# Performance work log

Hardware: AMD Instinct MI355X
Metric: run time of the kernel (lower is better)

Reference implementation:

```python
import jax, jax.numpy as jnp
import numpy as np

H = 16  # num_attention_heads
LN_EPS = 1e-12


def setup_inputs() -> dict:
    key = jax.random.key(0)
    ks = jax.random.split(key, 13)
    S, B, D = 2048, 2, 1024
    std = 0.02
    return {
        "query_tensor": jax.random.normal(ks[0], (S, B, D), jnp.float32),
        "key_tensor": jax.random.normal(ks[1], (S, B, D), jnp.float32),
        "value_tensor": jax.random.normal(ks[2], (S, B, D), jnp.float32),
        "Wq": jax.random.normal(ks[3], (D, D), jnp.float32) * std,
        "bq": jnp.zeros((D,), jnp.float32),
        "Wk": jax.random.normal(ks[4], (D, D), jnp.float32) * std,
        "bk": jnp.zeros((D,), jnp.float32),
        "Wv": jax.random.normal(ks[5], (D, D), jnp.float32) * std,
        "bv": jnp.zeros((D,), jnp.float32),
        "Wo": jax.random.normal(ks[6], (D, D), jnp.float32) * std,
        "bo": jnp.zeros((D,), jnp.float32),
        "ln_w": jnp.ones((D,), jnp.float32),
        "ln_b": jnp.zeros((D,), jnp.float32),
    }


def _layernorm(x, w, b):
    u = jnp.mean(x, axis=-1, keepdims=True)
    s = jnp.mean(jnp.square(x - u), axis=-1, keepdims=True)
    return w * ((x - u) / jnp.sqrt(s + LN_EPS)) + b


def reference(query_tensor, key_tensor, value_tensor, Wq, bq, Wk, bk, Wv, bv, Wo, bo, ln_w, ln_b):
    S, B, D = query_tensor.shape
    dh = D // H
    # QKV projections (nn.Linear: x @ W.T + b)
    q = query_tensor @ Wq.T + bq          # (S, B, D)
    k = key_tensor @ Wk.T + bk            # (Sk, B, D)
    v = value_tensor @ Wv.T + bv          # (Sk, B, D)
    # (S, B, D) -> (B*H, S, dh)
    q = q.reshape(S, B * H, dh).transpose(1, 0, 2)
    k = k.reshape(-1, B * H, dh).transpose(1, 0, 2)
    v = v.reshape(-1, B * H, dh).transpose(1, 0, 2)
    # NOTE: original code has NO 1/sqrt(dh) scaling
    scores = jnp.einsum('nqd,nkd->nqk', q, k)            # (B*H, S, Sk)
    probs = jax.nn.softmax(scores, axis=-1)
    # dropout is identity in eval mode
    ctx = jnp.einsum('nqk,nkd->nqd', probs, v)           # (B*H, S, dh)
    ctx = ctx.transpose(1, 0, 2).reshape(S, B, D)
    # BertSelfOutput: dense + residual + LayerNorm (dropout identity)
    out = ctx @ Wo.T + bo
    return _layernorm(out + query_tensor, ln_w, ln_b)
```

## Files before the change

### kernel.cpp

```cpp
#include <hip/hip_runtime.h>

#define SEQ    2048
#define BATCH  2
#define DMODEL 1024
#define NHEAD  16
#define DH     64
#define MROWS  (SEQ*BATCH)
#define RS     (BATCH*DMODEL)
#define LN_EPS 1e-12f

typedef __attribute__((ext_vector_type(8))) short short8;
typedef __attribute__((ext_vector_type(4))) float floatx4;

#define AS_GLOBAL __attribute__((address_space(1)))
#define AS_LDS    __attribute__((address_space(3)))

__device__ __forceinline__ float bf2f(unsigned short s) {
    union { unsigned u; float f; } a; a.u = ((unsigned)s) << 16; return a.f;
}
__device__ __forceinline__ unsigned short f2bf(float x) {
    union { float f; unsigned u; } a; a.f = x;
    unsigned r = a.u + 0x7fffu + ((a.u >> 16) & 1u);
    return (unsigned short)(r >> 16);
}
__device__ __forceinline__ uint4 cvt8(const float* __restrict__ p) {
    float4 x0 = *(const float4*)(p);
    float4 x1 = *(const float4*)(p + 4);
    union { uint4 u; unsigned short s[8]; } r;
    r.s[0] = f2bf(x0.x); r.s[1] = f2bf(x0.y);
    r.s[2] = f2bf(x0.z); r.s[3] = f2bf(x0.w);
    r.s[4] = f2bf(x1.x); r.s[5] = f2bf(x1.y);
    r.s[6] = f2bf(x1.z); r.s[7] = f2bf(x1.w);
    return r.u;
}

__global__ void beacon_kernel(float* out, float val) {
    if (threadIdx.x == 0) out[0] = val;
}

__global__ __launch_bounds__(256)
void cvt_kernel(const float* __restrict__ s0, const float* __restrict__ s1,
                const float* __restrict__ s2, const float* __restrict__ s3,
                const float* __restrict__ s4, const float* __restrict__ s5,
                const float* __restrict__ s6,
                unsigned short* __restrict__ d0, unsigned short* __restrict__ d1,
                unsigned short* __restrict__ d2, unsigned short* __restrict__ d3,
                unsigned short* __restrict__ d4, unsigned short* __restrict__ d5,
                unsigned short* __restrict__ d6)
{
    const float* srcs[7] = {s0, s1, s2, s3, s4, s5, s6};
    unsigned short* dsts[7] = {d0, d1, d2, d3, d4, d5, d6};
    const int cnts[7] = {4194304, 4194304, 4194304, 1048576, 1048576, 1048576, 1048576};
    const int z = blockIdx.z;
    const float* src = srcs[z];
    unsigned short* dst = dsts[z];
    const int count = cnts[z];
    const int stride = gridDim.x * 256 * 8;
    for (int i = (blockIdx.x * 256 + threadIdx.x) * 8; i < count; i += stride)
        *(uint4*)&dst[i] = cvt8(&src[i]);
}

__global__ __launch_bounds__(256)
void vt_kernel(const unsigned short* __restrict__ Vb,
               unsigned short* __restrict__ VT)
{
    __shared__ __align__(16) short T[64*72];
    const int tid = threadIdx.x;
    const int s0 = blockIdx.x * 64;
    const int bh = blockIdx.y;
    const int b = bh >> 4, h = bh & 15;

    #pragma unroll
    for (int rep = 0; rep < 2; ++rep) {
        int c = tid + rep * 256;
        int s = c >> 3, cc = c & 7;
        *(uint4*)&T[s*72 + cc*8] =
            *(const uint4*)&Vb[((s0 + s) * BATCH + b) * DMODEL + h*64 + cc*8];
    }
    __syncthreads();
    #pragma unroll
    for (int rep = 0; rep < 2; ++rep) {
        int o = tid + rep * 256;
        int d = o >> 3, sc = o & 7;
        union { uint4 u; unsigned short e[8]; } pk;
        #pragma unroll
        for (int j = 0; j < 8; ++j)
            pk.e[j] = (unsigned short)T[(sc*8 + j)*72 + d];
        *(uint4*)&VT[bh*(DH*SEQ) + d*SEQ + s0 + sc*8] = pk.u;
    }
}

template<int OUTF32>
__device__ __forceinline__ void gemm_bf16_body(
    const unsigned short* __restrict__ A,
    const unsigned short* __restrict__ W,
    const float* __restrict__ bias,
    void* __restrict__ Cout)
{
    __shared__ __align__(16) short Alds[128*32];
    __shared__ __align__(16) short Blds[128*32];

    const int tid  = threadIdx.x;
    const int lane = tid & 63;
    const int wave = tid >> 6;
    const int lrow = lane & 15;
    const int lq   = lane >> 4;
    const int m0 = blockIdx.x * 128;
    const int n0 = blockIdx.y * 128;
    const int mw = (wave >> 1) * 64;
    const int nw = (wave & 1) * 64;
    const int K  = DMODEL;

    const int chunk0 = tid;
    const int chunk1 = tid + 256;
    const int row0 = chunk0 >> 2, col0 = (chunk0 & 3) << 3;
    const int row1 = chunk1 >> 2, col1 = (chunk1 & 3) << 3;
    const unsigned short* gA0 = &A[(m0 + row0) * K + col0];
    const unsigned short* gA1 = &A[(m0 + row1) * K + col1];
    const unsigned short* gB0 = &W[(n0 + row0) * K + col0];
    const unsigned short* gB1 = &W[(n0 + row1) * K + col1];
    AS_LDS unsigned int* lA0 = (AS_LDS unsigned int*)&Alds[(wave*64)*8];
    AS_LDS unsigned int* lA1 = (AS_LDS unsigned int*)&Alds[(256 + wave*64)*8];
    AS_LDS unsigned int* lB0 = (AS_LDS unsigned int*)&Blds[(wave*64)*8];
    AS_LDS unsigned int* lB1 = (AS_LDS unsigned int*)&Blds[(256 + wave*64)*8];

    floatx4 zero = {0.f, 0.f, 0.f, 0.f};
    floatx4 acc[4][4];
    #pragma unroll
    for (int i = 0; i < 4; ++i)
        #pragma unroll
        for (int j = 0; j < 4; ++j) acc[i][j] = zero;

    for (int k0 = 0; k0 < K; k0 += 32) {
        __builtin_amdgcn_global_load_lds((const AS_GLOBAL unsigned int*)(gA0 + k0), lA0, 16, 0, 0);
        __builtin_amdgcn_global_load_lds((const AS_GLOBAL unsigned int*)(gA1 + k0), lA1, 16, 0, 0);
        __builtin_amdgcn_global_load_lds((const AS_GLOBAL unsigned int*)(gB0 + k0), lB0, 16, 0, 0);
        __builtin_amdgcn_global_load_lds((const AS_GLOBAL unsigned int*)(gB1 + k0), lB1, 16, 0, 0);
        __syncthreads();
        short8 af[4], bfg[4];
        #pragma unroll
        for (int mi = 0; mi < 4; ++mi)
            af[mi] = *(const short8*)&Alds[(mw + mi*16 + lrow)*32 + lq*8];
        #pragma unroll
        for (int ni = 0; ni < 4; ++ni)
            bfg[ni] = *(const short8*)&Blds[(nw + ni*16 + lrow)*32 + lq*8];
        #pragma unroll
        for (int mi = 0; mi < 4; ++mi)
            #pragma unroll
            for (int ni = 0; ni < 4; ++ni)
                acc[mi][ni] = __builtin_amdgcn_mfma_f32_16x16x32_bf16(af[mi], bfg[ni], acc[mi][ni], 0, 0, 0);
        __syncthreads();
    }

    #pragma unroll
    for (int mi = 0; mi < 4; ++mi) {
        #pragma unroll
        for (int ni = 0; ni < 4; ++ni) {
            int n = n0 + nw + ni*16 + lrow;
            float bv_ = bias[n];
            #pragma unroll
            for (int r = 0; r < 4; ++r) {
                int m = m0 + mw + mi*16 + lq*4 + r;
                float v = acc[mi][ni][r] + bv_;
                if (OUTF32) ((float*)Cout)[m * DMODEL + n] = v;
                else ((unsigned short*)Cout)[m * DMODEL + n] = f2bf(v);
            }
        }
    }
}

__global__ __launch_bounds__(256)
void qkv_bf16(const unsigned short* __restrict__ qb, const unsigned short* __restrict__ kb,
              const unsigned short* __restrict__ vb,
              const unsigned short* __restrict__ Wqb, const float* __restrict__ bq,
              const unsigned short* __restrict__ Wkb, const float* __restrict__ bk,
              const unsigned short* __restrict__ Wvb, const float* __restrict__ bv,
              unsigned short* __restrict__ Qo, unsigned short* __restrict__ Ko,
              unsigned short* __restrict__ Vo)
{
    const unsigned short *A, *W; const float* B; unsigned short* C;
    if (blockIdx.z == 0)      { A = qb; W = Wqb; B = bq; C = Qo; }
    else if (blockIdx.z == 1) { A = kb; W = Wkb; B = bk; C = Ko; }
    else                      { A = vb; W = Wvb; B = bv; C = Vo; }
    gemm_bf16_body<0>(A, W, B, C);
}

__global__ __launch_bounds__(256)
void oproj_bf16(const unsigned short* __restrict__ Cx,
                const unsigned short* __restrict__ Wob, const float* __restrict__ bo,
                float* __restrict__ O32)
{
    gemm_bf16_body<1>(Cx, Wob, bo, O32);
}

__global__ __launch_bounds__(256)
void qkv_mfma(const float* __restrict__ q_in, const float* __restrict__ k_in,
              const float* __restrict__ v_in,
              const float* __restrict__ Wq, const float* __restrict__ bq,
              const float* __restrict__ Wk, const float* __restrict__ bk,
              const float* __restrict__ Wv, const float* __restrict__ bv,
              unsigned short* __restrict__ Qo, unsigned short* __restrict__ Ko,
              unsigned short* __restrict__ Vo)
{
    const float *A, *W, *B; unsigned short* C;
    if (blockIdx.z == 0)      { A = q_in; W = Wq; B = bq; C = Qo; }
    else if (blockIdx.z == 1) { A = k_in; W = Wk; B = bk; C = Ko; }
    else                      { A = v_in; W = Wv; B = bv; C = Vo; }

    __shared__ __align__(16) short Alds[128*32];
    __shared__ __align__(16) short Blds[128*32];
    const int tid  = threadIdx.x;
    const int lane = tid & 63;
    const int wave = tid >> 6;
    const int lrow = lane & 15;
    const int lq   = lane >> 4;
    const int m0 = blockIdx.x * 128;
    const int n0 = blockIdx.y * 128;
    const int mw = (wave >> 1) * 64;
    const int nw = (wave & 1) * 64;
    const int K  = DMODEL;

    floatx4 zero = {0.f, 0.f, 0.f, 0.f};
    floatx4 acc[4][4];
    #pragma unroll
    for (int i = 0; i < 4; ++i)
        #pragma unroll
        for (int j = 0; j < 4; ++j) acc[i][j] = zero;

    for (int k0 = 0; k0 < K; k0 += 32) {
        #pragma unroll
        for (int rep = 0; rep < 2; ++rep) {
            int chunk = tid + rep * 256;
            int row = chunk >> 2;
            int col = (chunk & 3) << 3;
            *(uint4*)&Alds[row*32 + col] = cvt8(&A[(m0 + row) * K + k0 + col]);
            *(uint4*)&Blds[row*32 + col] = cvt8(&W[(n0 + row) * K + k0 + col]);
        }
        __syncthreads();
        short8 af[4], bfg[4];
        #pragma unroll
        for (int mi = 0; mi < 4; ++mi)
            af[mi] = *(const short8*)&Alds[(mw + mi*16 + lrow)*32 + lq*8];
        #pragma unroll
        for (int ni = 0; ni < 4; ++ni)
            bfg[ni] = *(const short8*)&Blds[(nw + ni*16 + lrow)*32 + lq*8];
        #pragma unroll
        for (int mi = 0; mi < 4; ++mi)
            #pragma unroll
            for (int ni = 0; ni < 4; ++ni)
                acc[mi][ni] = __builtin_amdgcn_mfma_f32_16x16x32_bf16(af[mi], bfg[ni], acc[mi][ni], 0, 0, 0);
        __syncthreads();
    }

    #pragma unroll
    for (int mi = 0; mi < 4; ++mi) {
        #pragma unroll
        for (int ni = 0; ni < 4; ++ni) {
            int n = n0 + nw + ni*16 + lrow;
            float bv_ = B[n];
            #pragma unroll
            for (int r = 0; r < 4; ++r) {
                int m = m0 + mw + mi*16 + lq*4 + r;
                C[m * DMODEL + n] = f2bf(acc[mi][ni][r] + bv_);
            }
        }
    }
}

__global__ __launch_bounds__(256)
void oproj_mfma(const unsigned short* __restrict__ Cx,
                const float* __restrict__ Wo, const float* __restrict__ bo,
                float* __restrict__ O32)
{
    __shared__ __align__(16) short Alds[128*32];
    __shared__ __align__(16) short Blds[128*32];
    const int tid  = threadIdx.x;
    const int lane = tid & 63;
    const int wave = tid >> 6;
    const int lrow = lane & 15;
    const int lq   = lane >> 4;
    const int m0 = blockIdx.x * 128;
    const int n0 = blockIdx.y * 128;
    const int mw = (wave >> 1) * 64;
    const int nw = (wave & 1) * 64;
    const int K  = DMODEL;

    floatx4 zero = {0.f, 0.f, 0.f, 0.f};
    floatx4 acc[4][4];
    #pragma unroll
    for (int i = 0; i < 4; ++i)
        #pragma unroll
        for (int j = 0; j < 4; ++j) acc[i][j] = zero;

    for (int k0 = 0; k0 < K; k0 += 32) {
        #pragma unroll
        for (int rep = 0; rep < 2; ++rep) {
            int chunk = tid + rep * 256;
            int row = chunk >> 2;
            int col = (chunk & 3) << 3;
            *(uint4*)&Alds[row*32 + col] = *(const uint4*)&Cx[(m0 + row) * K + k0 + col];
            *(uint4*)&Blds[row*32 + col] = cvt8(&Wo[(n0 + row) * K + k0 + col]);
        }
        __syncthreads();
        short8 af[4], bfg[4];
        #pragma unroll
        for (int mi = 0; mi < 4; ++mi)
            af[mi] = *(const short8*)&Alds[(mw + mi*16 + lrow)*32 + lq*8];
        #pragma unroll
        for (int ni = 0; ni < 4; ++ni)
            bfg[ni] = *(const short8*)&Blds[(nw + ni*16 + lrow)*32 + lq*8];
        #pragma unroll
        for (int mi = 0; mi < 4; ++mi)
            #pragma unroll
            for (int ni = 0; ni < 4; ++ni)
                acc[mi][ni] = __builtin_amdgcn_mfma_f32_16x16x32_bf16(af[mi], bfg[ni], acc[mi][ni], 0, 0, 0);
        __syncthreads();
    }

    #pragma unroll
    for (int mi = 0; mi < 4; ++mi) {
        #pragma unroll
        for (int ni = 0; ni < 4; ++ni) {
            int n = n0 + nw + ni*16 + lrow;
            float bv_ = bo[n];
            #pragma unroll
            for (int r = 0; r < 4; ++r) {
                int m = m0 + mw + mi*16 + lq*4 + r;
                O32[m * DMODEL + n] = acc[mi][ni][r] + bv_;
            }
        }
    }
}

__global__ __launch_bounds__(256)
void attn_mfma3(const unsigned short* __restrict__ Q,
                const unsigned short* __restrict__ Kg,
                const unsigned short* __restrict__ VT,
                unsigned short* __restrict__ Ctx)
{
    __shared__ __align__(16) short Qs[64*64];
    __shared__ __align__(16) short Ks[64*64];
    __shared__ __align__(16) short Vt[64*64];
    __shared__ __align__(16) short Ps[4][16*72];

    const int tid  = threadIdx.x;
    const int lane = tid & 63;
    const int wave = tid >> 6;
    const int lrow = lane & 15;
    const int lq   = lane >> 4;

    const int q0 = blockIdx.x * 64;
    const int bh = blockIdx.y;
    const int off = (bh >> 4) * DMODEL + (bh & 15) * DH;
    const unsigned short* VTb = VT + bh * (DH * SEQ);

    #pragma unroll
    for (int rep = 0; rep < 2; ++rep) {
        int c = rep*256 + wave*64 + lane;
        int r = c >> 3, cc = c & 7;
        const unsigned short* g = &Q[(q0 + r) * RS + off + ((cc ^ (r & 7)) << 3)];
        AS_LDS unsigned int* l = (AS_LDS unsigned int*)&Qs[(rep*256 + wave*64) * 8];
        __builtin_amdgcn_global_load_lds((const AS_GLOBAL unsigned int*)g, l, 16, 0, 0);
    }
    __syncthreads();

    short8 qf[2];
    #pragma unroll
    for (int ks = 0; ks < 2; ++ks) {
        int r = wave*16 + lrow;
        int cc = ks*4 + lq;
        qf[ks] = *(const short8*)&Qs[r*64 + ((cc ^ (r & 7)) << 3)];
    }

    floatx4 zero = {0.f, 0.f, 0.f, 0.f};
    float m_i = -1e30f, l_i = 0.f;
    floatx4 oacc[4];
    #pragma unroll
    for (int ni = 0; ni < 4; ++ni) oacc[ni] = zero;

    for (int kt = 0; kt < SEQ/64; ++kt) {
        __syncthreads();
        const int kbase = kt * 64;
        #pragma unroll
        for (int rep = 0; rep < 2; ++rep) {
            int c = rep*256 + wave*64 + lane;
            int r = c >> 3, cc = c & 7;
            int sw = ((cc ^ (r & 7)) << 3);
            const unsigned short* gk = &Kg[(kbase + r) * RS + off + sw];
            const unsigned short* gv = &VTb[r * SEQ + kbase + sw];
            AS_LDS unsigned int* lk = (AS_LDS unsigned int*)&Ks[(rep*256 + wave*64) * 8];
            AS_LDS unsigned int* lv = (AS_LDS unsigned int*)&Vt[(rep*256 + wave*64) * 8];
            __builtin_amdgcn_global_load_lds((const AS_GLOBAL unsigned int*)gk, lk, 16, 0, 0);
            __builtin_amdgcn_global_load_lds((const AS_GLOBAL unsigned int*)gv, lv, 16, 0, 0);
        }
        __syncthreads();

        floatx4 sacc[4];
        #pragma unroll
        for (int ni = 0; ni < 4; ++ni) sacc[ni] = zero;
        #pragma unroll
        for (int ni = 0; ni < 4; ++ni) {
            #pragma unroll
            for (int ks = 0; ks < 2; ++ks) {
                int key = ni*16 + lrow;
                int cc  = ks*4 + lq;
                short8 kf = *(const short8*)&Ks[key*64 + ((cc ^ (key & 7)) << 3)];
                sacc[ni] = __builtin_amdgcn_mfma_f32_16x16x32_bf16(kf, qf[ks], sacc[ni], 0, 0, 0);
            }
        }

        float mx = sacc[0][0];
        #pragma unroll
        for (int ni = 0; ni < 4; ++ni)
            #pragma unroll
            for (int r = 0; r < 4; ++r) mx = fmaxf(mx, sacc[ni][r]);
        mx = fmaxf(mx, __shfl_xor(mx, 16));
        mx = fmaxf(mx, __shfl_xor(mx, 32));
        float mnew = fmaxf(m_i, mx);
        float alpha = __expf(m_i - mnew);
        float p[4][4];
        float psum = 0.f;
        #pragma unroll
        for (int ni = 0; ni < 4; ++ni)
            #pragma unroll
            for (int r = 0; r < 4; ++r) {
                p[ni][r] = __expf(sacc[ni][r] - mnew);
                psum += p[ni][r];
            }
        psum += __shfl_xor(psum, 16);
        psum += __shfl_xor(psum, 32);
        l_i = l_i * alpha + psum;
        m_i = mnew;
        #pragma unroll
        for (int ni = 0; ni < 4; ++ni)
            #pragma unroll
            for (int r = 0; r < 4; ++r) oacc[ni][r] *= alpha;

        #pragma unroll
        for (int ni = 0; ni < 4; ++ni) {
            uint2 pk;
            pk.x = (unsigned)f2bf(p[ni][0]) | ((unsigned)f2bf(p[ni][1]) << 16);
            pk.y = (unsigned)f2bf(p[ni][2]) | ((unsigned)f2bf(p[ni][3]) << 16);
            *(uint2*)&Ps[wave][lrow*72 + ni*16 + lq*4] = pk;
        }
        __builtin_amdgcn_wave_barrier();

        short8 pf[2];
        #pragma unroll
        for (int ks = 0; ks < 2; ++ks)
            pf[ks] = *(const short8*)&Ps[wave][lrow*72 + ks*32 + lq*8];
        #pragma unroll
        for (int ni = 0; ni < 4; ++ni) {
            #pragma unroll
            for (int ks = 0; ks < 2; ++ks) {
                int d  = ni*16 + lrow;
                int cc = ks*4 + lq;
                short8 vf = *(const short8*)&Vt[d*64 + ((cc ^ (d & 7)) << 3)];
                oacc[ni] = __builtin_amdgcn_mfma_f32_16x16x32_bf16(vf, pf[ks], oacc[ni], 0, 0, 0);
            }
        }
    }

    const float inv = 1.f / l_i;
    const int q = q0 + wave*16 + lrow;
    #pragma unroll
    for (int ni = 0; ni < 4; ++ni) {
        uint2 ok;
        ok.x = (unsigned)f2bf(oacc[ni][0] * inv) | ((unsigned)f2bf(oacc[ni][1] * inv) << 16);
        ok.y = (unsigned)f2bf(oacc[ni][2] * inv) | ((unsigned)f2bf(oacc[ni][3] * inv) << 16);
        *(uint2*)&Ctx[q * RS + off + ni*16 + lq*4] = ok;
    }
}

__global__ __launch_bounds__(256)
void attn_mfma2(const unsigned short* __restrict__ Q,
                const unsigned short* __restrict__ Kg,
                const unsigned short* __restrict__ V,
                unsigned short* __restrict__ Ctx)
{
    __shared__ __align__(16) short Qs[64*72];
    __shared__ __align__(16) short Ks[64*72];
    __shared__ __align__(16) short Vt[64*72];
    __shared__ __align__(16) short Ps[4][16*72];

    const int tid  = threadIdx.x;
    const int lane = tid & 63;
    const int wave = tid >> 6;
    const int lrow = lane & 15;
    const int lq   = lane >> 4;

    const int q0 = blockIdx.x * 64;
    const int bh = blockIdx.y;
    const int off = (bh >> 4) * DMODEL + (bh & 15) * DH;

    #pragma unroll
    for (int rep = 0; rep < 2; ++rep) {
        int chunk = tid + rep * 256;
        int r = chunk >> 3;
        int c = (chunk & 7) << 3;
        *(uint4*)&Qs[r*72 + c] = *(const uint4*)&Q[(q0 + r) * RS + off + c];
    }
    __syncthreads();

    short8 qf[2];
    #pragma unroll
    for (int ks = 0; ks < 2; ++ks)
        qf[ks] = *(const short8*)&Qs[(wave*16 + lrow)*72 + ks*32 + lq*8];

    floatx4 zero = {0.f, 0.f, 0.f, 0.f};
    float m_i = -1e30f, l_i = 0.f;
    floatx4 oacc[4];
    #pragma unroll
    for (int ni = 0; ni < 4; ++ni) oacc[ni] = zero;

    for (int kt = 0; kt < SEQ/64; ++kt) {
        __syncthreads();
        const int kbase = kt * 64;
        #pragma unroll
        for (int rep = 0; rep < 2; ++rep) {
            int chunk = tid + rep * 256;
            int r = chunk >> 3;
            int c = (chunk & 7) << 3;
            *(uint4*)&Ks[r*72 + c] = *(const uint4*)&Kg[(kbase + r) * RS + off + c];
            uint4 vv = *(const uint4*)&V[(kbase + r) * RS + off + c];
            union { uint4 u; short s[8]; } uv; uv.u = vv;
            int swz = (chunk & 7) << 3;
            #pragma unroll
            for (int j = 0; j < 8; ++j)
                Vt[(c + j)*72 + (r ^ swz)] = uv.s[j];
        }
        __syncthreads();

        floatx4 sacc[4];
        #pragma unroll
        for (int ni = 0; ni < 4; ++ni) sacc[ni] = zero;
        #pragma unroll
        for (int ni = 0; ni < 4; ++ni) {
            #pragma unroll
            for (int ks = 0; ks < 2; ++ks) {
                short8 kf = *(const short8*)&Ks[(ni*16 + lrow)*72 + ks*32 + lq*8];
                sacc[ni] = __builtin_amdgcn_mfma_f32_16x16x32_bf16(kf, qf[ks], sacc[ni], 0, 0, 0);
            }
        }

        float mx = sacc[0][0];
        #pragma unroll
        for (int ni = 0; ni < 4; ++ni)
            #pragma unroll
            for (int r = 0; r < 4; ++r) mx = fmaxf(mx, sacc[ni][r]);
        mx = fmaxf(mx, __shfl_xor(mx, 16));
        mx = fmaxf(mx, __shfl_xor(mx, 32));
        float mnew = fmaxf(m_i, mx);
        float alpha = __expf(m_i - mnew);
        float p[4][4];
        float psum = 0.f;
        #pragma unroll
        for (int ni = 0; ni < 4; ++ni)
            #pragma unroll
            for (int r = 0; r < 4; ++r) {
                p[ni][r] = __expf(sacc[ni][r] - mnew);
                psum += p[ni][r];
            }
        psum += __shfl_xor(psum, 16);
        psum += __shfl_xor(psum, 32);
        l_i = l_i * alpha + psum;
        m_i = mnew;
        #pragma unroll
        for (int ni = 0; ni < 4; ++ni)
            #pragma unroll
            for (int r = 0; r < 4; ++r) oacc[ni][r] *= alpha;

        #pragma unroll
        for (int ni = 0; ni < 4; ++ni) {
            uint2 pk;
            pk.x = (unsigned)f2bf(p[ni][0]) | ((unsigned)f2bf(p[ni][1]) << 16);
            pk.y = (unsigned)f2bf(p[ni][2]) | ((unsigned)f2bf(p[ni][3]) << 16);
            *(uint2*)&Ps[wave][lrow*72 + ni*16 + lq*4] = pk;
        }
        __builtin_amdgcn_wave_barrier();

        short8 pf[2];
        #pragma unroll
        for (int ks = 0; ks < 2; ++ks)
            pf[ks] = *(const short8*)&Ps[wave][lrow*72 + ks*32 + lq*8];
        #pragma unroll
        for (int ni = 0; ni < 4; ++ni) {
            #pragma unroll
            for (int ks = 0; ks < 2; ++ks) {
                int d  = ni*16 + lrow;
                int kk = ks*32 + lq*8;
                int swz = ((d >> 3) & 7) << 3;
                short8 vf = *(const short8*)&Vt[d*72 + (kk ^ swz)];
                oacc[ni] = __builtin_amdgcn_mfma_f32_16x16x32_bf16(vf, pf[ks], oacc[ni], 0, 0, 0);
            }
        }
    }

    const float inv = 1.f / l_i;
    const int q = q0 + wave*16 + lrow;
    #pragma unroll
    for (int ni = 0; ni < 4; ++ni) {
        uint2 ok;
        ok.x = (unsigned)f2bf(oacc[ni][0] * inv) | ((unsigned)f2bf(oacc[ni][1] * inv) << 16);
        ok.y = (unsigned)f2bf(oacc[ni][2] * inv) | ((unsigned)f2bf(oacc[ni][3] * inv) << 16);
        *(uint2*)&Ctx[q * RS + off + ni*16 + lq*4] = ok;
    }
}

__global__ __launch_bounds__(256)
void ln2_kernel(const float* __restrict__ O,
                const float* __restrict__ resid,
                const float* __restrict__ w,
                const float* __restrict__ bb,
                float* __restrict__ out)
{
    __shared__ float r1[256];
    __shared__ float r2[256];
    const int row = blockIdx.x;
    const int tid = threadIdx.x;
    const int c4 = tid * 4;

    float4 o4 = *(const float4*)&O[row * DMODEL + c4];
    float4 q4 = *(const float4*)&resid[row * DMODEL + c4];
    float x0 = o4.x + q4.x;
    float x1 = o4.y + q4.y;
    float x2 = o4.z + q4.z;
    float x3 = o4.w + q4.w;

    r1[tid] = x0 + x1 + x2 + x3;
    r2[tid] = x0*x0 + x1*x1 + x2*x2 + x3*x3;
    __syncthreads();
    for (int st = 128; st > 0; st >>= 1) {
        if (tid < st) { r1[tid] += r1[tid + st]; r2[tid] += r2[tid + st]; }
        __syncthreads();
    }
    const float mean = r1[0] * (1.f / DMODEL);
    float var = r2[0] * (1.f / DMODEL) - mean * mean;
    var = fmaxf(var, 0.f);
    const float rstd = rsqrtf(var + LN_EPS);

    float4 w4 = *(const float4*)&w[c4];
    float4 b4 = *(const float4*)&bb[c4];
    float4 y;
    y.x = w4.x * ((x0 - mean) * rstd) + b4.x;
    y.y = w4.y * ((x1 - mean) * rstd) + b4.y;
    y.z = w4.z * ((x2 - mean) * rstd) + b4.z;
    y.w = w4.w * ((x3 - mean) * rstd) + b4.w;
    *(float4*)&out[row * DMODEL + c4] = y;
}

extern "C" void kernel_launch(void* const* d_in, const int* in_sizes, int n_in,
                              void* d_out, int out_size, void* d_ws, size_t ws_size,
                              hipStream_t stream) {
    const float* q_in = (const float*)d_in[0];
    const float* k_in = (const float*)d_in[1];
    const float* v_in = (const float*)d_in[2];
    const float* Wq = (const float*)d_in[3];  const float* bq = (const float*)d_in[4];
    const float* Wk = (const float*)d_in[5];  const float* bk = (const float*)d_in[6];
    const float* Wv = (const float*)d_in[7];  const float* bv = (const float*)d_in[8];
    const float* Wo = (const float*)d_in[9];  const float* bo = (const float*)d_in[10];
    const float* lnw = (const float*)d_in[11]; const float* lnb = (const float*)d_in[12];

    char* wsb = (char*)d_ws;
    unsigned short* QCtx = (unsigned short*)d_out;
    float*          outF = (float*)d_out;
    dim3 blk(256);

    if (ws_size >= (48u << 20)) {
        unsigned short* qb  = (unsigned short*)(wsb);
        unsigned short* kb  = (unsigned short*)(wsb + (8u  << 20));
        unsigned short* vb  = (unsigned short*)(wsb + (16u << 20));
        unsigned short* Wqb = (unsigned short*)(wsb + (24u << 20));
        unsigned short* Wkb = (unsigned short*)(wsb + (26u << 20));
        unsigned short* Wvb = (unsigned short*)(wsb + (28u << 20));
        unsigned short* Wob = (unsigned short*)(wsb + (30u << 20));
        unsigned short* Kb  = (unsigned short*)(wsb + (32u << 20));
        unsigned short* Vb  = (unsigned short*)(wsb + (40u << 20));
        unsigned short* VT  = (unsigned short*)(wsb);
        float*          O32 = (float*)(wsb);

        cvt_kernel<<<dim3(512, 1, 7), blk, 0, stream>>>(
            q_in, k_in, v_in, Wq, Wk, Wv, Wo,
            qb, kb, vb, Wqb, Wkb, Wvb, Wob);
        qkv_bf16<<<dim3(MROWS/128, DMODEL/128, 3), blk, 0, stream>>>(
            qb, kb, vb, Wqb, bq, Wkb, bk, Wvb, bv, QCtx, Kb, Vb);
        vt_kernel<<<dim3(SEQ/64, BATCH*NHEAD), blk, 0, stream>>>(Vb, VT);
        attn_mfma3<<<dim3(SEQ/64, BATCH*NHEAD), blk, 0, stream>>>(QCtx, Kb, VT, QCtx);
        oproj_bf16<<<dim3(MROWS/128, DMODEL/128), blk, 0, stream>>>(QCtx, Wob, bo, O32);
        ln2_kernel<<<dim3(MROWS), blk, 0, stream>>>(O32, q_in, lnw, lnb, outF);
    } else if (ws_size >= (16u << 20)) {
        unsigned short* Kb  = (unsigned short*)(wsb);
        unsigned short* Vb  = (unsigned short*)(wsb + (8u << 20));
        float*          O32 = (float*)(wsb);
        qkv_mfma<<<dim3(MROWS/128, DMODEL/128, 3), blk, 0, stream>>>(
            q_in, k_in, v_in, Wq, bq, Wk, bk, Wv, bv, QCtx, Kb, Vb);
        attn_mfma2<<<dim3(SEQ/64, BATCH*NHEAD), blk, 0, stream>>>(QCtx, Kb, Vb, QCtx);
        oproj_mfma<<<dim3(MROWS/128, DMODEL/128), blk, 0, stream>>>(QCtx, Wo, bo, O32);
        ln2_kernel<<<dim3(MROWS), blk, 0, stream>>>(O32, q_in, lnw, lnb, outF);
    } else {
        beacon_kernel<<<1, 64, 0, stream>>>((float*)d_out, 300.0f);
    }
}
```

Before: 271.1 us.

## Double-buffer K/V tiles in attention with lazy softmax rescale and shuffle LayerNorm

The attention kernel now double-buffers K and V^T tiles in LDS and prefetches the next tile before computing on the current one, leaving one barrier per iteration. This is meant to hide global-load latency behind the MFMA work. It also loads Q fragments straight from global memory and skips the online-softmax rescale unless the running max grows by more than 8. It further uses the hardware packed bf16 convert, swizzles the P scratch buffer, and raises wave priority around the MFMA blocks. LayerNorm replaces its LDS tree reduction with wave shuffles; the trade-offs are more LDS per block (about 40KB) and exp values up to e^8 before normalisation.

```diff
diff --git a/kernel.cpp b/kernel.cpp
--- a/kernel.cpp
+++ b/kernel.cpp
@@ -22,6 +22,11 @@
     union { float f; unsigned u; } a; a.f = x;
     unsigned r = a.u + 0x7fffu + ((a.u >> 16) & 1u);
     return (unsigned short)(r >> 16);
+}
+__device__ __forceinline__ unsigned cvt_pk_bf16(float a, float b) {
+    unsigned r;
+    asm("v_cvt_pk_bf16_f32 %0, %1, %2" : "=v"(r) : "v"(a), "v"(b));
+    return r;
 }
 __device__ __forceinline__ uint4 cvt8(const float* __restrict__ p) {
     float4 x0 = *(const float4*)(p);
@@ -333,15 +338,12 @@
 }
 
 __global__ __launch_bounds__(256)
-void attn_mfma3(const unsigned short* __restrict__ Q,
+void attn_mfma4(const unsigned short* __restrict__ Q,
                 const unsigned short* __restrict__ Kg,
                 const unsigned short* __restrict__ VT,
                 unsigned short* __restrict__ Ctx)
 {
-    __shared__ __align__(16) short Qs[64*64];
-    __shared__ __align__(16) short Ks[64*64];
-    __shared__ __align__(16) short Vt[64*64];
-    __shared__ __align__(16) short Ps[4][16*72];
+    __shared__ __align__(16) short SMEM[20480];
 
     const int tid  = threadIdx.x;
     const int lane = tid & 63;
@@ -353,24 +355,32 @@
     const int bh = blockIdx.y;
     const int off = (bh >> 4) * DMODEL + (bh & 15) * DH;
     const unsigned short* VTb = VT + bh * (DH * SEQ);
-
-    #pragma unroll
-    for (int rep = 0; rep < 2; ++rep) {
-        int c = rep*256 + wave*64 + lane;
-        int r = c >> 3, cc = c & 7;
-        const unsigned short* g = &Q[(q0 + r) * RS + off + ((cc ^ (r & 7)) << 3)];
-        AS_LDS unsigned int* l = (AS_LDS unsigned int*)&Qs[(rep*256 + wave*64) * 8];
-        __builtin_amdgcn_global_load_lds((const AS_GLOBAL unsigned int*)g, l, 16, 0, 0);
-    }
-    __syncthreads();
-
+    short* const psw = &SMEM[16384 + wave * 1024];
+
+    auto stageKV = [&](int kt, int b) {
+        const int kbase = kt * 64;
+        short* ksb = &SMEM[b * 8192];
+        short* vtb = &SMEM[b * 8192 + 4096];
+        #pragma unroll
+        for (int rep = 0; rep < 2; ++rep) {
+            int c = rep*256 + tid;
+            int r = c >> 3, cc = c & 7;
+            int sw = ((cc ^ (r & 7)) << 3);
+            __builtin_amdgcn_global_load_lds(
+                (const AS_GLOBAL unsigned int*)&Kg[(kbase + r) * RS + off + sw],
+                (AS_LDS unsigned int*)&ksb[(rep*256 + wave*64) * 8], 16, 0, 0);
+            __builtin_amdgcn_global_load_lds(
+                (const AS_GLOBAL unsigned int*)&VTb[r * SEQ + kbase + sw],
+                (AS_LDS unsigned int*)&vtb[(rep*256 + wave*64) * 8], 16, 0, 0);
+        }
+    };
+
+    stageKV(0, 0);
+
+    const int qrow = q0 + wave*16 + lrow;
     short8 qf[2];
-    #pragma unroll
-    for (int ks = 0; ks < 2; ++ks) {
-        int r = wave*16 + lrow;
-        int cc = ks*4 + lq;
-        qf[ks] = *(const short8*)&Qs[r*64 + ((cc ^ (r & 7)) << 3)];
-    }
+    qf[0] = *(const short8*)&Q[qrow * RS + off + lq*8];
+    qf[1] = *(const short8*)&Q[qrow * RS + off + 32 + lq*8];
 
     floatx4 zero = {0.f, 0.f, 0.f, 0.f};
     float m_i = -1e30f, l_i = 0.f;
@@ -378,36 +388,29 @@
     #pragma unroll
     for (int ni = 0; ni < 4; ++ni) oacc[ni] = zero;
 
+    __syncthreads();
+
     for (int kt = 0; kt < SEQ/64; ++kt) {
-        __syncthreads();
-        const int kbase = kt * 64;
-        #pragma unroll
-        for (int rep = 0; rep < 2; ++rep) {
-            int c = rep*256 + wave*64 + lane;
-            int r = c >> 3, cc = c & 7;
-            int sw = ((cc ^ (r & 7)) << 3);
-            const unsigned short* gk = &Kg[(kbase + r) * RS + off + sw];
-            const unsigned short* gv = &VTb[r * SEQ + kbase + sw];
-            AS_LDS unsigned int* lk = (AS_LDS unsigned int*)&Ks[(rep*256 + wave*64) * 8];
-            AS_LDS unsigned int* lv = (AS_LDS unsigned int*)&Vt[(rep*256 + wave*64) * 8];
-            __builtin_amdgcn_global_load_lds((const AS_GLOBAL unsigned int*)gk, lk, 16, 0, 0);
-            __builtin_amdgcn_global_load_lds((const AS_GLOBAL unsigned int*)gv, lv, 16, 0, 0);
-        }
-        __syncthreads();
+        const int cur = kt & 1;
+        if (kt + 1 < SEQ/64) stageKV(kt + 1, cur ^ 1);
+        const short* ksb = &SMEM[cur * 8192];
+        const short* vtb = &SMEM[cur * 8192 + 4096];
 
         floatx4 sacc[4];
         #pragma unroll
         for (int ni = 0; ni < 4; ++ni) sacc[ni] = zero;
-        #pragma unroll
-        for (int ni = 0; ni < 4; ++ni) {
-            #pragma unroll
-            for (int ks = 0; ks < 2; ++ks) {
+        __builtin_amdgcn_s_setprio(1);
+        #pragma unroll
+        for (int ni = 0; ni < 4; ++ni) {
+            #pragma unroll
+            for (int kk = 0; kk < 2; ++kk) {
                 int key = ni*16 + lrow;
-                int cc  = ks*4 + lq;
-                short8 kf = *(const short8*)&Ks[key*64 + ((cc ^ (key & 7)) << 3)];
-                sacc[ni] = __builtin_amdgcn_mfma_f32_16x16x32_bf16(kf, qf[ks], sacc[ni], 0, 0, 0);
-            }
-        }
+                int cc  = kk*4 + lq;
+                short8 kf = *(const short8*)&ksb[key*64 + ((cc ^ (key & 7)) << 3)];
+                sacc[ni] = __builtin_amdgcn_mfma_f32_16x16x32_bf16(kf, qf[kk], sacc[ni], 0, 0, 0);
+            }
+        }
+        __builtin_amdgcn_s_setprio(0);
 
         float mx = sacc[0][0];
         #pragma unroll
@@ -416,59 +419,71 @@
             for (int r = 0; r < 4; ++r) mx = fmaxf(mx, sacc[ni][r]);
         mx = fmaxf(mx, __shfl_xor(mx, 16));
         mx = fmaxf(mx, __shfl_xor(mx, 32));
-        float mnew = fmaxf(m_i, mx);
-        float alpha = __expf(m_i - mnew);
+        if (!__all(mx <= m_i + 8.f)) {
+            float mnew = fmaxf(m_i, mx);
+            float alpha = __expf(m_i - mnew);
+            l_i *= alpha;
+            #pragma unroll
+            for (int ni = 0; ni < 4; ++ni)
+                #pragma unroll
+                for (int r = 0; r < 4; ++r) oacc[ni][r] *= alpha;
+            m_i = mnew;
+        }
         float p[4][4];
         float psum = 0.f;
         #pragma unroll
         for (int ni = 0; ni < 4; ++ni)
             #pragma unroll
             for (int r = 0; r < 4; ++r) {
-                p[ni][r] = __expf(sacc[ni][r] - mnew);
+                p[ni][r] = __expf(sacc[ni][r] - m_i);
                 psum += p[ni][r];
             }
         psum += __shfl_xor(psum, 16);
         psum += __shfl_xor(psum, 32);
-        l_i = l_i * alpha + psum;
-        m_i = mnew;
-        #pragma unroll
-        for (int ni = 0; ni < 4; ++ni)
-            #pragma unroll
-            for (int r = 0; r < 4; ++r) oacc[ni][r] *= alpha;
+        l_i += psum;
 
         #pragma unroll
         for (int ni = 0; ni < 4; ++ni) {
             uint2 pk;
-            pk.x = (unsigned)f2bf(p[ni][0]) | ((unsigned)f2bf(p[ni][1]) << 16);
-            pk.y = (unsigned)f2bf(p[ni][2]) | ((unsigned)f2bf(p[ni][3]) << 16);
-            *(uint2*)&Ps[wave][lrow*72 + ni*16 + lq*4] = pk;
+            pk.x = cvt_pk_bf16(p[ni][0], p[ni][1]);
+            pk.y = cvt_pk_bf16(p[ni][2], p[ni][3]);
+            int t  = ni*2 + (lq >> 1);
+            int tp = t ^ (lrow & 7);
+            *(uint2*)&psw[lrow*64 + tp*8 + (lq & 1)*4] = pk;
         }
         __builtin_amdgcn_wave_barrier();
 
         short8 pf[2];
         #pragma unroll
-        for (int ks = 0; ks < 2; ++ks)
-            pf[ks] = *(const short8*)&Ps[wave][lrow*72 + ks*32 + lq*8];
-        #pragma unroll
-        for (int ni = 0; ni < 4; ++ni) {
-            #pragma unroll
-            for (int ks = 0; ks < 2; ++ks) {
+        for (int kk = 0; kk < 2; ++kk) {
+            int t  = kk*4 + lq;
+            int tp = t ^ (lrow & 7);
+            pf[kk] = *(const short8*)&psw[lrow*64 + tp*8];
+        }
+
+        __builtin_amdgcn_s_setprio(1);
+        #pragma unroll
+        for (int ni = 0; ni < 4; ++ni) {
+            #pragma unroll
+            for (int kk = 0; kk < 2; ++kk) {
                 int d  = ni*16 + lrow;
-                int cc = ks*4 + lq;
-                short8 vf = *(const short8*)&Vt[d*64 + ((cc ^ (d & 7)) << 3)];
-                oacc[ni] = __builtin_amdgcn_mfma_f32_16x16x32_bf16(vf, pf[ks], oacc[ni], 0, 0, 0);
-            }
-        }
+                int cc = kk*4 + lq;
+                short8 vf = *(const short8*)&vtb[d*64 + ((cc ^ (d & 7)) << 3)];
+                oacc[ni] = __builtin_amdgcn_mfma_f32_16x16x32_bf16(vf, pf[kk], oacc[ni], 0, 0, 0);
+            }
+        }
+        __builtin_amdgcn_s_setprio(0);
+
+        __syncthreads();
     }
 
     const float inv = 1.f / l_i;
-    const int q = q0 + wave*16 + lrow;
     #pragma unroll
     for (int ni = 0; ni < 4; ++ni) {
         uint2 ok;
-        ok.x = (unsigned)f2bf(oacc[ni][0] * inv) | ((unsigned)f2bf(oacc[ni][1] * inv) << 16);
-        ok.y = (unsigned)f2bf(oacc[ni][2] * inv) | ((unsigned)f2bf(oacc[ni][3] * inv) << 16);
-        *(uint2*)&Ctx[q * RS + off + ni*16 + lq*4] = ok;
+        ok.x = cvt_pk_bf16(oacc[ni][0] * inv, oacc[ni][1] * inv);
+        ok.y = cvt_pk_bf16(oacc[ni][2] * inv, oacc[ni][3] * inv);
+        *(uint2*)&Ctx[qrow * RS + off + ni*16 + lq*4] = ok;
     }
 }
 
@@ -614,8 +629,8 @@
                 const float* __restrict__ bb,
                 float* __restrict__ out)
 {
-    __shared__ float r1[256];
-    __shared__ float r2[256];
+    __shared__ float r1s[4];
+    __shared__ float r2s[4];
     const int row = blockIdx.x;
     const int tid = threadIdx.x;
     const int c4 = tid * 4;
@@ -627,15 +642,20 @@
     float x2 = o4.z + q4.z;
     float x3 = o4.w + q4.w;
 
-    r1[tid] = x0 + x1 + x2 + x3;
-    r2[tid] = x0*x0 + x1*x1 + x2*x2 + x3*x3;
+    float s1 = x0 + x1 + x2 + x3;
+    float s2 = x0*x0 + x1*x1 + x2*x2 + x3*x3;
+    #pragma unroll
+    for (int o = 32; o > 0; o >>= 1) {
+        s1 += __shfl_xor(s1, o);
+        s2 += __shfl_xor(s2, o);
+    }
+    if ((tid & 63) == 0) { r1s[tid >> 6] = s1; r2s[tid >> 6] = s2; }
     __syncthreads();
-    for (int st = 128; st > 0; st >>= 1) {
-        if (tid < st) { r1[tid] += r1[tid + st]; r2[tid] += r2[tid + st]; }
-        __syncthreads();
-    }
-    const float mean = r1[0] * (1.f / DMODEL);
-    float var = r2[0] * (1.f / DMODEL) - mean * mean;
+    float t1 = r1s[0] + r1s[1] + r1s[2] + r1s[3];
+    float t2 = r2s[0] + r2s[1] + r2s[2] + r2s[3];
+
+    const float mean = t1 * (1.f / DMODEL);
+    float var = t2 * (1.f / DMODEL) - mean * mean;
     var = fmaxf(var, 0.f);
     const float rstd = rsqrtf(var + LN_EPS);
 
@@ -685,7 +705,7 @@
         qkv_bf16<<<dim3(MROWS/128, DMODEL/128, 3), blk, 0, stream>>>(
             qb, kb, vb, Wqb, bq, Wkb, bk, Wvb, bv, QCtx, Kb, Vb);
         vt_kernel<<<dim3(SEQ/64, BATCH*NHEAD), blk, 0, stream>>>(Vb, VT);
-        attn_mfma3<<<dim3(SEQ/64, BATCH*NHEAD), blk, 0, stream>>>(QCtx, Kb, VT, QCtx);
+        attn_mfma4<<<dim3(SEQ/64, BATCH*NHEAD), blk, 0, stream>>>(QCtx, Kb, VT, QCtx);
         oproj_bf16<<<dim3(MROWS/128, DMODEL/128), blk, 0, stream>>>(QCtx, Wob, bo, O32);
         ln2_kernel<<<dim3(MROWS), blk, 0, stream>>>(O32, q_in, lnw, lnb, outF);
     } else if (ws_size >= (16u << 20)) {
```

New measurement: 256.8 us. -5.3%, faster.
